# Performance work log

Hardware: AMD Instinct MI355X
Metric: run time of the kernel (lower is better)

The kernel has to match this reference:

```python
import jax, jax.numpy as jnp
import numpy as np

GAMMA = 0.99
EPS = 1e-8
N = 16777216  # flattened reward count


def setup_inputs() -> dict:
    key = jax.random.key(0)
    rewards = jax.random.normal(key, (N,), dtype=jnp.float32)
    return {"rewards": rewards}


def reference(rewards):
    # Sequential recurrence: R_t = gamma*R_{t-1} + r_t, Welford stats over R_t,
    # scaled[i] = r_i / max(std_t, eps), std_t = sqrt(var_sum/count) (1.0 if count < 2).
    flat = rewards.reshape(-1)

    def step(carry, r):
        R, cnt, mean, var_sum = carry
        R = GAMMA * R + r
        cnt = cnt + 1.0
        delta = R - mean
        mean = mean + delta / cnt
        var_sum = var_sum + delta * (R - mean)
        std = jnp.where(cnt < 2.0, jnp.float32(1.0), jnp.sqrt(var_sum / cnt))
        std = jnp.maximum(std, jnp.float32(EPS))
        return (R, cnt, mean, var_sum), r / std

    init = (jnp.float32(0.0), jnp.float32(0.0), jnp.float32(0.0), jnp.float32(0.0))
    _, scaled = jax.lax.scan(step, init, flat)
    return scaled.reshape(rewards.shape)
```

## Files before the change

kernel.cpp:

```cpp
#include <hip/hip_runtime.h>
#include <math.h>

#define THREADS 256
#define GAMMA 0.99

typedef float vf4 __attribute__((ext_vector_type(4)));

__device__ __forceinline__ int padi16(int i) { return i + (i >> 4); }

template<int NW>
__device__ __forceinline__ void block_compose_excl(int tid, double g, double v,
                                                   double& eg, double& ev,
                                                   double* lg, double* lv) {
    const int lane = tid & 63, wave = tid >> 6;
    double ig = g, iv = v;
#pragma unroll
    for (int k = 1; k < 64; k <<= 1) {
        double og = __shfl_up(ig, k);
        double ov = __shfl_up(iv, k);
        if (lane >= k) { iv = fma(ig, ov, iv); ig *= og; }
    }
    double weg = __shfl_up(ig, 1);
    double wev = __shfl_up(iv, 1);
    if (lane == 0) { weg = 1.0; wev = 0.0; }
    if (lane == 63) { lg[wave] = ig; lv[wave] = iv; }
    __syncthreads();
    double bg = 1.0, bv = 0.0;
    for (int w = 0; w < wave; ++w) { bv = fma(lg[w], bv, lv[w]); bg *= lg[w]; }
    eg = weg * bg;
    ev = fma(weg, bv, wev);
}

template<int NW>
__device__ __forceinline__ void block_add_excl2(int tid, double a, double b,
                                                double& ea, double& eb,
                                                double* la, double* lb) {
    const int lane = tid & 63, wave = tid >> 6;
    double ia = a, ib = b;
#pragma unroll
    for (int k = 1; k < 64; k <<= 1) {
        double oa = __shfl_up(ia, k);
        double ob = __shfl_up(ib, k);
        if (lane >= k) { ia += oa; ib += ob; }
    }
    double wea = __shfl_up(ia, 1);
    double web = __shfl_up(ib, 1);
    if (lane == 0) { wea = 0.0; web = 0.0; }
    if (lane == 63) { la[wave] = ia; lb[wave] = ib; }
    __syncthreads();
    double ba = 0.0, bb = 0.0;
    for (int w = 0; w < wave; ++w) { ba += la[w]; bb += lb[w]; }
    ea = wea + ba;
    eb = web + bb;
}


__global__ __launch_bounds__(THREADS) void w_phase1(const float* __restrict__ in,
                                                    vf4* __restrict__ aggf,
                                                    double* __restrict__ bagg, int nw) {
    __shared__ double sA[4], sPs[4], sPq[4], sP2[4];
    const int tid = threadIdx.x, lane = tid & 63, w = tid >> 6;
    const int wid = blockIdx.x * 4 + w;

    const float* src = in + (size_t)wid * 1024 + (size_t)lane * 16;
    float rv[16];
#pragma unroll
    for (int q = 0; q < 4; ++q) {
        const float4 t = ((const float4*)src)[q];
        rv[4 * q] = t.x; rv[4 * q + 1] = t.y; rv[4 * q + 2] = t.z; rv[4 * q + 3] = t.w;
    }
    const float gf = (float)GAMMA;
    float p = 0.f, psum = 0.f, pq = 0.f, p2 = 0.f, gp = 1.f;
#pragma unroll
    for (int j = 0; j < 16; ++j) {
        p = fmaf(gf, p, rv[j]);
        gp *= gf;
        psum += p;
        pq = fmaf(gp, p, pq);
        p2 = fmaf(p, p, p2);
    }
    const double g = GAMMA;
    double gPT = g;
#pragma unroll
    for (int e = 0; e < 4; ++e) gPT *= gPT;

    float ig = (float)gPT, iv = p;
#pragma unroll
    for (int k = 1; k < 64; k <<= 1) {
        float og = __shfl_up(ig, k);
        float ov = __shfl_up(iv, k);
        if (lane >= k) { iv = fmaf(ig, ov, iv); ig *= og; }
    }
    float rho = __shfl_up(iv, 1), gexc = __shfl_up(ig, 1);
    if (lane == 0) { rho = 0.f; gexc = 1.f; }
    const float A = __shfl(iv, 63);

    const float G1f = (float)(g * (1.0 - gPT) / (1.0 - g));
    const float G2f = (float)(g * g * (1.0 - gPT * gPT) / (1.0 - g * g));
    float c1 = fmaf(rho, G1f, psum);
    float c2 = gexc * fmaf(rho, G2f, pq);
    float c3 = fmaf(rho * rho, G2f, fmaf(2.f * rho, pq, p2));
#pragma unroll
    for (int k = 32; k > 0; k >>= 1) {
        c1 += __shfl_down(c1, k);
        c2 += __shfl_down(c2, k);
        c3 += __shfl_down(c3, k);
    }
    if (lane == 0) {
        vf4 a; a.x = A; a.y = c1; a.z = c2; a.w = c3;
        aggf[wid] = a;
        sA[w] = (double)A; sPs[w] = (double)c1; sPq[w] = (double)c2; sP2[w] = (double)c3;
    }
    __syncthreads();
    if (tid == 0) {
        double gC = g;
#pragma unroll
        for (int e = 0; e < 10; ++e) gC *= gC;
        const double G1C = g * (1.0 - gC) / (1.0 - g);
        const double G2C = g * g * (1.0 - gC * gC) / (1.0 - g * g);
        double Rin = 0.0, Ps = 0.0, Pq = 0.0, P2 = 0.0, gex = 1.0;
#pragma unroll
        for (int i = 0; i < 4; ++i) {
            Ps += fma(Rin, G1C, sPs[i]);
            Pq += gex * fma(Rin, G2C, sPq[i]);
            P2 += fma(Rin * Rin, G2C, fma(2.0 * Rin, sPq[i], sP2[i]));
            Rin = fma(gC, Rin, sA[i]);
            gex *= gC;
        }
        bagg[4 * (size_t)blockIdx.x + 0] = Rin;
        bagg[4 * (size_t)blockIdx.x + 1] = Ps;
        bagg[4 * (size_t)blockIdx.x + 2] = Pq;
        bagg[4 * (size_t)blockIdx.x + 3] = P2;
    }
}

template<int CPT, int LOG2CHUNK>
__global__ __launch_bounds__(1024) void rs_phase2(const double* __restrict__ agg,
                                                  double* __restrict__ car, int nchunk) {
    __shared__ double lg[16], lv[16], la[16], lb[16];
    const int t = threadIdx.x;
    const double g = GAMMA;
    double gC = g;
#pragma unroll
    for (int e = 0; e < LOG2CHUNK; ++e) gC *= gC;

    double A[CPT], Ps[CPT], Pq[CPT], P2[CPT];
    const int c0 = t * CPT;
#pragma unroll
    for (int i = 0; i < CPT; ++i) {
        const int c = c0 + i;
        const bool ok = c < nchunk;
        A[i]  = ok ? agg[4 * (size_t)c + 0] : 0.0;
        Ps[i] = ok ? agg[4 * (size_t)c + 1] : 0.0;
        Pq[i] = ok ? agg[4 * (size_t)c + 2] : 0.0;
        P2[i] = ok ? agg[4 * (size_t)c + 3] : 0.0;
    }
    double mg = 1.0, mv = 0.0;
#pragma unroll
    for (int i = 0; i < CPT; ++i) { mv = fma(gC, mv, A[i]); mg *= gC; }

    double eg, ev;
    block_compose_excl<16>(t, mg, mv, eg, ev, lg, lv);

    const double G1C = g * (1.0 - gC) / (1.0 - g);
    const double G2C = g * g * (1.0 - gC * gC) / (1.0 - g * g);
    double Rin[CPT + 1];
    Rin[0] = ev;
    double s1[CPT], s2[CPT];
#pragma unroll
    for (int i = 0; i < CPT; ++i) {
        s1[i] = fma(Rin[i], G1C, Ps[i]);
        s2[i] = fma(Rin[i] * Rin[i], G2C, fma(2.0 * Rin[i], Pq[i], P2[i]));
        Rin[i + 1] = fma(gC, Rin[i], A[i]);
    }
    double ts1 = 0.0, ts2 = 0.0;
#pragma unroll
    for (int i = 0; i < CPT; ++i) { ts1 += s1[i]; ts2 += s2[i]; }
    double ea, eb;
    block_add_excl2<16>(t, ts1, ts2, ea, eb, la, lb);
#pragma unroll
    for (int i = 0; i < CPT; ++i) {
        const int c = c0 + i;
        if (c < nchunk) {
            car[3 * (size_t)c + 0] = Rin[i];
            car[3 * (size_t)c + 1] = ea;
            car[3 * (size_t)c + 2] = eb;
        }
        ea += s1[i];
        eb += s2[i];
    }
}

__global__ __launch_bounds__(THREADS) void w_expand(const double* __restrict__ bcar,
                                                    const vf4* __restrict__ aggf,
                                                    double* __restrict__ wcar, int nc) {
    const int c = blockIdx.x * THREADS + threadIdx.x;
    if (c >= nc) return;
    const double g = GAMMA;
    double gW = g;
#pragma unroll
    for (int e = 0; e < 10; ++e) gW *= gW;
    const double G1W = g * (1.0 - gW) / (1.0 - g);
    const double G2W = g * g * (1.0 - gW * gW) / (1.0 - g * g);

    const vf4 a0 = aggf[4 * (size_t)c + 0];
    const vf4 a1 = aggf[4 * (size_t)c + 1];
    const vf4 a2 = aggf[4 * (size_t)c + 2];
    const vf4 a3 = aggf[4 * (size_t)c + 3];
    double wR  = bcar[3 * (size_t)c + 0];
    double wS1 = bcar[3 * (size_t)c + 1];
    double wS2 = bcar[3 * (size_t)c + 2];

    const vf4 aj[4] = {a0, a1, a2, a3};
#pragma unroll
    for (int j = 0; j < 4; ++j) {
        const size_t wd = 4 * (size_t)c + j;
        wcar[3 * wd + 0] = wR;
        wcar[3 * wd + 1] = wS1;
        wcar[3 * wd + 2] = wS2;
        const double Aw = (double)aj[j].x, Pw = (double)aj[j].y;
        const double Qw = (double)aj[j].z, Sw = (double)aj[j].w;
        wS1 += fma(wR, G1W, Pw);
        wS2 += fma(wR * wR, G2W, fma(2.0 * wR, Qw, Sw));
        wR = fma(gW, wR, Aw);
    }
}

__global__ __launch_bounds__(THREADS) void w_phase3(const float* __restrict__ in,
                                                    float* __restrict__ out,
                                                    const double* __restrict__ wcar, int nw) {
    __shared__ float sbuf[THREADS / 64][1024 + 64];
    const int tid = threadIdx.x, lane = tid & 63, w = tid >> 6;
    const int wid = blockIdx.x * 4 + w;

    const double RinC = wcar[3 * (size_t)wid + 0];
    const double S1C  = wcar[3 * (size_t)wid + 1];
    const double S2C  = wcar[3 * (size_t)wid + 2];

    const float* src = in + (size_t)wid * 1024 + (size_t)lane * 16;
    float rv[16];
#pragma unroll
    for (int q = 0; q < 4; ++q) {
        const float4 t = ((const float4*)src)[q];
        rv[4 * q] = t.x; rv[4 * q + 1] = t.y; rv[4 * q + 2] = t.z; rv[4 * q + 3] = t.w;
    }
    const float gf = (float)GAMMA;
    float p = 0.f, psum = 0.f, pq = 0.f, p2 = 0.f, gp = 1.f;
#pragma unroll
    for (int j = 0; j < 16; ++j) {
        p = fmaf(gf, p, rv[j]);
        gp *= gf;
        psum += p;
        pq = fmaf(gp, p, pq);
        p2 = fmaf(p, p, p2);
    }
    const double g = GAMMA;
    double gPT = g;
#pragma unroll
    for (int e = 0; e < 4; ++e) gPT *= gPT;

    if (wid == 0) {
        double ig = gPT, iv = (double)p;
#pragma unroll
        for (int k = 1; k < 64; k <<= 1) {
            double og = __shfl_up(ig, k);
            double ov = __shfl_up(iv, k);
            if (lane >= k) { iv = fma(ig, ov, iv); ig *= og; }
        }
        double rho = __shfl_up(iv, 1), gexc = __shfl_up(ig, 1);
        if (lane == 0) { rho = 0.0; gexc = 1.0; }
        const double rin = fma(gexc, RinC, rho);
        const double G1 = g * (1.0 - gPT) / (1.0 - g);
        const double G2 = g * g * (1.0 - gPT * gPT) / (1.0 - g * g);
        double s1 = fma(rin, G1, (double)psum);
        double s2 = fma(rin * rin, G2, fma(2.0 * rin, (double)pq, (double)p2));
        double ia = s1, ib = s2;
#pragma unroll
        for (int k = 1; k < 64; k <<= 1) {
            double oa = __shfl_up(ia, k);
            double ob = __shfl_up(ib, k);
            if (lane >= k) { ia += oa; ib += ob; }
        }
        double ea = __shfl_up(ia, 1), eb = __shfl_up(ib, 1);
        if (lane == 0) { ea = 0.0; eb = 0.0; }
        double R = rin, S1 = S1C + ea, S2 = S2C + eb;
        const int a0 = lane * 17;
        const size_t gbase = (size_t)lane * 16;
        for (int j = 0; j < 16; ++j) {
            const float rf = rv[j];
            R = fma(g, R, (double)rf);
            S1 += R;
            S2 = fma(R, R, S2);
            float ov;
            if (gbase + j == 0) {
                ov = rf;
            } else {
                const double cnt = (double)(gbase + j + 1);
                const double inv = 1.0 / cnt;
                const double mean = S1 * inv;
                double var = fma(S2, inv, -(mean * mean));
                var = var > 0.0 ? var : 0.0;
                double sd = sqrt(var);
                sd = sd > 1e-8 ? sd : 1e-8;
                ov = (float)((double)rf / sd);
            }
            sbuf[w][a0 + j] = ov;
        }
    } else {
        float ig = (float)gPT, iv = p;
#pragma unroll
        for (int k = 1; k < 64; k <<= 1) {
            float og = __shfl_up(ig, k);
            float ov = __shfl_up(iv, k);
            if (lane >= k) { iv = fmaf(ig, ov, iv); ig *= og; }
        }
        float rho = __shfl_up(iv, 1), gexc = __shfl_up(ig, 1);
        if (lane == 0) { rho = 0.f; gexc = 1.f; }
        const float rin = fmaf(gexc, (float)RinC, rho);
        const float G1f = (float)(g * (1.0 - gPT) / (1.0 - g));
        const float G2f = (float)(g * g * (1.0 - gPT * gPT) / (1.0 - g * g));
        float s1 = fmaf(rin, G1f, psum);
        float s2 = fmaf(rin * rin, G2f, fmaf(2.f * rin, pq, p2));
        float ia = s1, ib = s2;
#pragma unroll
        for (int k = 1; k < 64; k <<= 1) {
            float oa = __shfl_up(ia, k);
            float ob = __shfl_up(ib, k);
            if (lane >= k) { ia += oa; ib += ob; }
        }
        float ea = __shfl_up(ia, 1), eb = __shfl_up(ib, 1);
        if (lane == 0) { ea = 0.f; eb = 0.f; }
        const float S1bf = (float)S1C + ea;
        const float S2bf = (float)S2C + eb;

        float R = rin;
        float ls1 = 0.f, ls2 = 0.f;
        const float base_cnt = (float)((size_t)wid * 1024 + (size_t)lane * 16);
        const int a0 = lane * 17;
#pragma unroll
        for (int j = 0; j < 16; ++j) {
            const float rf = rv[j];
            R = fmaf(gf, R, rf);
            ls1 += R;
            ls2 = fmaf(R, R, ls2);
            const float cnt = base_cnt + (float)(j + 1);
            const float S1f = S1bf + ls1;
            const float S2f = S2bf + ls2;
            float t = fmaf(S2f, cnt, -(S1f * S1f));
            t = fmaxf(t, 1e-12f);
            sbuf[w][a0 + j] = rf * cnt * __builtin_amdgcn_rsqf(t);
        }
    }

    asm volatile("s_waitcnt lgkmcnt(0)" ::: "memory");

    float* dst = out + (size_t)wid * 1024;
#pragma unroll
    for (int k = 0; k < 4; ++k) {
        const int i = lane * 4 + k * 256;
        const int pp = padi16(i);
        vf4 v;
        v.x = sbuf[w][pp]; v.y = sbuf[w][pp + 1]; v.z = sbuf[w][pp + 2]; v.w = sbuf[w][pp + 3];
        __builtin_nontemporal_store(v, (vf4*)(dst + i));
    }
}

extern "C" void kernel_launch(void* const* d_in, const int* in_sizes, int n_in,
                              void* d_out, int out_size, void* d_ws, size_t ws_size,
                              hipStream_t stream) {
    (void)n_in; (void)out_size; (void)ws_size;
    const float* in = (const float*)d_in[0];
    float* out = (float*)d_out;
    double* ws = (double*)d_ws;
    const int n = in_sizes[0];

    const int nw = n >> 10;
    const int nc = nw >> 2;
    double* bagg = ws;
    double* bcar = bagg + 4 * (size_t)nc;
    double* wcar = bcar + 3 * (size_t)nc;
    vf4* aggf = (vf4*)(wcar + 3 * (size_t)nw);

    w_phase1<<<nc, THREADS, 0, stream>>>(in, aggf, bagg, nw);
    rs_phase2<4, 12><<<1, 1024, 0, stream>>>(bagg, bcar, nc);
    w_expand<<<(nc + THREADS - 1) / THREADS, THREADS, 0, stream>>>(bcar, aggf, wcar, nc);
    w_phase3<<<nc, THREADS, 0, stream>>>(in, out, wcar, nw);
}
```

Measured before the change: 53.71 us.

## Fold warp-carry expansion into phase3 and move first-warp exact path to phase1

```diff
diff --git a/kernel.cpp b/kernel.cpp
--- a/kernel.cpp
+++ b/kernel.cpp
@@ -56,6 +56,7 @@
 
 
 __global__ __launch_bounds__(THREADS) void w_phase1(const float* __restrict__ in,
+                                                    float* __restrict__ out,
                                                     vf4* __restrict__ aggf,
                                                     double* __restrict__ bagg, int nw) {
     __shared__ double sA[4], sPs[4], sPq[4], sP2[4];
@@ -132,144 +133,17 @@
         bagg[4 * (size_t)blockIdx.x + 2] = Pq;
         bagg[4 * (size_t)blockIdx.x + 3] = P2;
     }
-}
-
-template<int CPT, int LOG2CHUNK>
-__global__ __launch_bounds__(1024) void rs_phase2(const double* __restrict__ agg,
-                                                  double* __restrict__ car, int nchunk) {
-    __shared__ double lg[16], lv[16], la[16], lb[16];
-    const int t = threadIdx.x;
-    const double g = GAMMA;
-    double gC = g;
-#pragma unroll
-    for (int e = 0; e < LOG2CHUNK; ++e) gC *= gC;
-
-    double A[CPT], Ps[CPT], Pq[CPT], P2[CPT];
-    const int c0 = t * CPT;
-#pragma unroll
-    for (int i = 0; i < CPT; ++i) {
-        const int c = c0 + i;
-        const bool ok = c < nchunk;
-        A[i]  = ok ? agg[4 * (size_t)c + 0] : 0.0;
-        Ps[i] = ok ? agg[4 * (size_t)c + 1] : 0.0;
-        Pq[i] = ok ? agg[4 * (size_t)c + 2] : 0.0;
-        P2[i] = ok ? agg[4 * (size_t)c + 3] : 0.0;
-    }
-    double mg = 1.0, mv = 0.0;
-#pragma unroll
-    for (int i = 0; i < CPT; ++i) { mv = fma(gC, mv, A[i]); mg *= gC; }
-
-    double eg, ev;
-    block_compose_excl<16>(t, mg, mv, eg, ev, lg, lv);
-
-    const double G1C = g * (1.0 - gC) / (1.0 - g);
-    const double G2C = g * g * (1.0 - gC * gC) / (1.0 - g * g);
-    double Rin[CPT + 1];
-    Rin[0] = ev;
-    double s1[CPT], s2[CPT];
-#pragma unroll
-    for (int i = 0; i < CPT; ++i) {
-        s1[i] = fma(Rin[i], G1C, Ps[i]);
-        s2[i] = fma(Rin[i] * Rin[i], G2C, fma(2.0 * Rin[i], Pq[i], P2[i]));
-        Rin[i + 1] = fma(gC, Rin[i], A[i]);
-    }
-    double ts1 = 0.0, ts2 = 0.0;
-#pragma unroll
-    for (int i = 0; i < CPT; ++i) { ts1 += s1[i]; ts2 += s2[i]; }
-    double ea, eb;
-    block_add_excl2<16>(t, ts1, ts2, ea, eb, la, lb);
-#pragma unroll
-    for (int i = 0; i < CPT; ++i) {
-        const int c = c0 + i;
-        if (c < nchunk) {
-            car[3 * (size_t)c + 0] = Rin[i];
-            car[3 * (size_t)c + 1] = ea;
-            car[3 * (size_t)c + 2] = eb;
-        }
-        ea += s1[i];
-        eb += s2[i];
-    }
-}
-
-__global__ __launch_bounds__(THREADS) void w_expand(const double* __restrict__ bcar,
-                                                    const vf4* __restrict__ aggf,
-                                                    double* __restrict__ wcar, int nc) {
-    const int c = blockIdx.x * THREADS + threadIdx.x;
-    if (c >= nc) return;
-    const double g = GAMMA;
-    double gW = g;
-#pragma unroll
-    for (int e = 0; e < 10; ++e) gW *= gW;
-    const double G1W = g * (1.0 - gW) / (1.0 - g);
-    const double G2W = g * g * (1.0 - gW * gW) / (1.0 - g * g);
-
-    const vf4 a0 = aggf[4 * (size_t)c + 0];
-    const vf4 a1 = aggf[4 * (size_t)c + 1];
-    const vf4 a2 = aggf[4 * (size_t)c + 2];
-    const vf4 a3 = aggf[4 * (size_t)c + 3];
-    double wR  = bcar[3 * (size_t)c + 0];
-    double wS1 = bcar[3 * (size_t)c + 1];
-    double wS2 = bcar[3 * (size_t)c + 2];
-
-    const vf4 aj[4] = {a0, a1, a2, a3};
-#pragma unroll
-    for (int j = 0; j < 4; ++j) {
-        const size_t wd = 4 * (size_t)c + j;
-        wcar[3 * wd + 0] = wR;
-        wcar[3 * wd + 1] = wS1;
-        wcar[3 * wd + 2] = wS2;
-        const double Aw = (double)aj[j].x, Pw = (double)aj[j].y;
-        const double Qw = (double)aj[j].z, Sw = (double)aj[j].w;
-        wS1 += fma(wR, G1W, Pw);
-        wS2 += fma(wR * wR, G2W, fma(2.0 * wR, Qw, Sw));
-        wR = fma(gW, wR, Aw);
-    }
-}
-
-__global__ __launch_bounds__(THREADS) void w_phase3(const float* __restrict__ in,
-                                                    float* __restrict__ out,
-                                                    const double* __restrict__ wcar, int nw) {
-    __shared__ float sbuf[THREADS / 64][1024 + 64];
-    const int tid = threadIdx.x, lane = tid & 63, w = tid >> 6;
-    const int wid = blockIdx.x * 4 + w;
-
-    const double RinC = wcar[3 * (size_t)wid + 0];
-    const double S1C  = wcar[3 * (size_t)wid + 1];
-    const double S2C  = wcar[3 * (size_t)wid + 2];
-
-    const float* src = in + (size_t)wid * 1024 + (size_t)lane * 16;
-    float rv[16];
-#pragma unroll
-    for (int q = 0; q < 4; ++q) {
-        const float4 t = ((const float4*)src)[q];
-        rv[4 * q] = t.x; rv[4 * q + 1] = t.y; rv[4 * q + 2] = t.z; rv[4 * q + 3] = t.w;
-    }
-    const float gf = (float)GAMMA;
-    float p = 0.f, psum = 0.f, pq = 0.f, p2 = 0.f, gp = 1.f;
-#pragma unroll
-    for (int j = 0; j < 16; ++j) {
-        p = fmaf(gf, p, rv[j]);
-        gp *= gf;
-        psum += p;
-        pq = fmaf(gp, p, pq);
-        p2 = fmaf(p, p, p2);
-    }
-    const double g = GAMMA;
-    double gPT = g;
-#pragma unroll
-    for (int e = 0; e < 4; ++e) gPT *= gPT;
-
-    if (wid == 0) {
-        double ig = gPT, iv = (double)p;
+
+    if (blockIdx.x == 0 && w == 0) {
+        double ig64 = gPT, iv64 = (double)p;
 #pragma unroll
         for (int k = 1; k < 64; k <<= 1) {
-            double og = __shfl_up(ig, k);
-            double ov = __shfl_up(iv, k);
-            if (lane >= k) { iv = fma(ig, ov, iv); ig *= og; }
-        }
-        double rho = __shfl_up(iv, 1), gexc = __shfl_up(ig, 1);
-        if (lane == 0) { rho = 0.0; gexc = 1.0; }
-        const double rin = fma(gexc, RinC, rho);
+            double og = __shfl_up(ig64, k);
+            double ov = __shfl_up(iv64, k);
+            if (lane >= k) { iv64 = fma(ig64, ov, iv64); ig64 *= og; }
+        }
+        double rin = __shfl_up(iv64, 1);
+        if (lane == 0) rin = 0.0;
         const double G1 = g * (1.0 - gPT) / (1.0 - g);
         const double G2 = g * g * (1.0 - gPT * gPT) / (1.0 - g * g);
         double s1 = fma(rin, G1, (double)psum);
@@ -283,8 +157,7 @@
         }
         double ea = __shfl_up(ia, 1), eb = __shfl_up(ib, 1);
         if (lane == 0) { ea = 0.0; eb = 0.0; }
-        double R = rin, S1 = S1C + ea, S2 = S2C + eb;
-        const int a0 = lane * 17;
+        double R = rin, S1 = ea, S2 = eb;
         const size_t gbase = (size_t)lane * 16;
         for (int j = 0; j < 16; ++j) {
             const float rf = rv[j];
@@ -304,52 +177,160 @@
                 sd = sd > 1e-8 ? sd : 1e-8;
                 ov = (float)((double)rf / sd);
             }
-            sbuf[w][a0 + j] = ov;
-        }
-    } else {
-        float ig = (float)gPT, iv = p;
-#pragma unroll
-        for (int k = 1; k < 64; k <<= 1) {
-            float og = __shfl_up(ig, k);
-            float ov = __shfl_up(iv, k);
-            if (lane >= k) { iv = fmaf(ig, ov, iv); ig *= og; }
-        }
-        float rho = __shfl_up(iv, 1), gexc = __shfl_up(ig, 1);
-        if (lane == 0) { rho = 0.f; gexc = 1.f; }
-        const float rin = fmaf(gexc, (float)RinC, rho);
-        const float G1f = (float)(g * (1.0 - gPT) / (1.0 - g));
-        const float G2f = (float)(g * g * (1.0 - gPT * gPT) / (1.0 - g * g));
-        float s1 = fmaf(rin, G1f, psum);
-        float s2 = fmaf(rin * rin, G2f, fmaf(2.f * rin, pq, p2));
-        float ia = s1, ib = s2;
-#pragma unroll
-        for (int k = 1; k < 64; k <<= 1) {
-            float oa = __shfl_up(ia, k);
-            float ob = __shfl_up(ib, k);
-            if (lane >= k) { ia += oa; ib += ob; }
-        }
-        float ea = __shfl_up(ia, 1), eb = __shfl_up(ib, 1);
-        if (lane == 0) { ea = 0.f; eb = 0.f; }
-        const float S1bf = (float)S1C + ea;
-        const float S2bf = (float)S2C + eb;
-
-        float R = rin;
-        float ls1 = 0.f, ls2 = 0.f;
-        const float base_cnt = (float)((size_t)wid * 1024 + (size_t)lane * 16);
-        const int a0 = lane * 17;
-#pragma unroll
-        for (int j = 0; j < 16; ++j) {
-            const float rf = rv[j];
-            R = fmaf(gf, R, rf);
-            ls1 += R;
-            ls2 = fmaf(R, R, ls2);
-            const float cnt = base_cnt + (float)(j + 1);
-            const float S1f = S1bf + ls1;
-            const float S2f = S2bf + ls2;
-            float t = fmaf(S2f, cnt, -(S1f * S1f));
-            t = fmaxf(t, 1e-12f);
-            sbuf[w][a0 + j] = rf * cnt * __builtin_amdgcn_rsqf(t);
-        }
+            out[gbase + j] = ov;
+        }
+    }
+}
+
+template<int CPT, int LOG2CHUNK>
+__global__ __launch_bounds__(1024) void rs_phase2(const double* __restrict__ agg,
+                                                  double* __restrict__ car, int nchunk) {
+    __shared__ double lg[16], lv[16], la[16], lb[16];
+    const int t = threadIdx.x;
+    const double g = GAMMA;
+    double gC = g;
+#pragma unroll
+    for (int e = 0; e < LOG2CHUNK; ++e) gC *= gC;
+
+    double A[CPT], Ps[CPT], Pq[CPT], P2[CPT];
+    const int c0 = t * CPT;
+#pragma unroll
+    for (int i = 0; i < CPT; ++i) {
+        const int c = c0 + i;
+        const bool ok = c < nchunk;
+        A[i]  = ok ? agg[4 * (size_t)c + 0] : 0.0;
+        Ps[i] = ok ? agg[4 * (size_t)c + 1] : 0.0;
+        Pq[i] = ok ? agg[4 * (size_t)c + 2] : 0.0;
+        P2[i] = ok ? agg[4 * (size_t)c + 3] : 0.0;
+    }
+    double mg = 1.0, mv = 0.0;
+#pragma unroll
+    for (int i = 0; i < CPT; ++i) { mv = fma(gC, mv, A[i]); mg *= gC; }
+
+    double eg, ev;
+    block_compose_excl<16>(t, mg, mv, eg, ev, lg, lv);
+
+    const double G1C = g * (1.0 - gC) / (1.0 - g);
+    const double G2C = g * g * (1.0 - gC * gC) / (1.0 - g * g);
+    double Rin[CPT + 1];
+    Rin[0] = ev;
+    double s1[CPT], s2[CPT];
+#pragma unroll
+    for (int i = 0; i < CPT; ++i) {
+        s1[i] = fma(Rin[i], G1C, Ps[i]);
+        s2[i] = fma(Rin[i] * Rin[i], G2C, fma(2.0 * Rin[i], Pq[i], P2[i]));
+        Rin[i + 1] = fma(gC, Rin[i], A[i]);
+    }
+    double ts1 = 0.0, ts2 = 0.0;
+#pragma unroll
+    for (int i = 0; i < CPT; ++i) { ts1 += s1[i]; ts2 += s2[i]; }
+    double ea, eb;
+    block_add_excl2<16>(t, ts1, ts2, ea, eb, la, lb);
+#pragma unroll
+    for (int i = 0; i < CPT; ++i) {
+        const int c = c0 + i;
+        if (c < nchunk) {
+            car[3 * (size_t)c + 0] = Rin[i];
+            car[3 * (size_t)c + 1] = ea;
+            car[3 * (size_t)c + 2] = eb;
+        }
+        ea += s1[i];
+        eb += s2[i];
+    }
+}
+
+__global__ __launch_bounds__(THREADS) void w_phase3(const float* __restrict__ in,
+                                                    float* __restrict__ out,
+                                                    const double* __restrict__ bcar,
+                                                    const vf4* __restrict__ aggf, int nw) {
+    __shared__ float sbuf[THREADS / 64][1024 + 64];
+    const int tid = threadIdx.x, lane = tid & 63, w = tid >> 6;
+    const int wid = blockIdx.x * 4 + w;
+    if (wid == 0) return;
+    const int b = blockIdx.x;
+
+    const float* src = in + (size_t)wid * 1024 + (size_t)lane * 16;
+    float rv[16];
+#pragma unroll
+    for (int q = 0; q < 4; ++q) {
+        const float4 t = ((const float4*)src)[q];
+        rv[4 * q] = t.x; rv[4 * q + 1] = t.y; rv[4 * q + 2] = t.z; rv[4 * q + 3] = t.w;
+    }
+
+    const double g = GAMMA;
+    double gW64 = g;
+#pragma unroll
+    for (int e = 0; e < 10; ++e) gW64 *= gW64;
+    const float gW  = (float)gW64;
+    const float G1W = (float)(g * (1.0 - gW64) / (1.0 - g));
+    const float G2W = (float)(g * g * (1.0 - gW64 * gW64) / (1.0 - g * g));
+
+    float Rc  = (float)bcar[3 * (size_t)b + 0];
+    float S1C = (float)bcar[3 * (size_t)b + 1];
+    float S2C = (float)bcar[3 * (size_t)b + 2];
+    for (int i = 0; i < w; ++i) {
+        const vf4 a = aggf[4 * (size_t)b + i];
+        S1C += fmaf(Rc, G1W, a.y);
+        S2C += fmaf(Rc * Rc, G2W, fmaf(2.f * Rc, a.z, a.w));
+        Rc = fmaf(gW, Rc, a.x);
+    }
+
+    const float gf = (float)GAMMA;
+    float p = 0.f, psum = 0.f, pq = 0.f, p2 = 0.f, gp = 1.f;
+#pragma unroll
+    for (int j = 0; j < 16; ++j) {
+        p = fmaf(gf, p, rv[j]);
+        gp *= gf;
+        psum += p;
+        pq = fmaf(gp, p, pq);
+        p2 = fmaf(p, p, p2);
+    }
+    double gPT64 = g;
+#pragma unroll
+    for (int e = 0; e < 4; ++e) gPT64 *= gPT64;
+
+    float ig = (float)gPT64, iv = p;
+#pragma unroll
+    for (int k = 1; k < 64; k <<= 1) {
+        float og = __shfl_up(ig, k);
+        float ov = __shfl_up(iv, k);
+        if (lane >= k) { iv = fmaf(ig, ov, iv); ig *= og; }
+    }
+    float rho = __shfl_up(iv, 1), gexc = __shfl_up(ig, 1);
+    if (lane == 0) { rho = 0.f; gexc = 1.f; }
+    const float rin = fmaf(gexc, Rc, rho);
+    const float G1f = (float)(g * (1.0 - gPT64) / (1.0 - g));
+    const float G2f = (float)(g * g * (1.0 - gPT64 * gPT64) / (1.0 - g * g));
+    float s1 = fmaf(rin, G1f, psum);
+    float s2 = fmaf(rin * rin, G2f, fmaf(2.f * rin, pq, p2));
+    float ia = s1, ib = s2;
+#pragma unroll
+    for (int k = 1; k < 64; k <<= 1) {
+        float oa = __shfl_up(ia, k);
+        float ob = __shfl_up(ib, k);
+        if (lane >= k) { ia += oa; ib += ob; }
+    }
+    float ea = __shfl_up(ia, 1), eb = __shfl_up(ib, 1);
+    if (lane == 0) { ea = 0.f; eb = 0.f; }
+    const float S1bf = S1C + ea;
+    const float S2bf = S2C + eb;
+
+    float R = rin;
+    float ls1 = 0.f, ls2 = 0.f;
+    const float base_cnt = (float)((size_t)wid * 1024 + (size_t)lane * 16);
+    const int a0 = lane * 17;
+#pragma unroll
+    for (int j = 0; j < 16; ++j) {
+        const float rf = rv[j];
+        R = fmaf(gf, R, rf);
+        ls1 += R;
+        ls2 = fmaf(R, R, ls2);
+        const float cnt = base_cnt + (float)(j + 1);
+        const float S1f = S1bf + ls1;
+        const float S2f = S2bf + ls2;
+        float t = fmaf(S2f, cnt, -(S1f * S1f));
+        t = fmaxf(t, 1e-12f);
+        sbuf[w][a0 + j] = rf * cnt * __builtin_amdgcn_rsqf(t);
     }
 
     asm volatile("s_waitcnt lgkmcnt(0)" ::: "memory");
@@ -378,11 +359,9 @@
     const int nc = nw >> 2;
     double* bagg = ws;
     double* bcar = bagg + 4 * (size_t)nc;
-    double* wcar = bcar + 3 * (size_t)nc;
-    vf4* aggf = (vf4*)(wcar + 3 * (size_t)nw);
-
-    w_phase1<<<nc, THREADS, 0, stream>>>(in, aggf, bagg, nw);
+    vf4* aggf = (vf4*)(bcar + 3 * (size_t)nc);
+
+    w_phase1<<<nc, THREADS, 0, stream>>>(in, out, aggf, bagg, nw);
     rs_phase2<4, 12><<<1, 1024, 0, stream>>>(bagg, bcar, nc);
-    w_expand<<<(nc + THREADS - 1) / THREADS, THREADS, 0, stream>>>(bcar, aggf, wcar, nc);
-    w_phase3<<<nc, THREADS, 0, stream>>>(in, out, wcar, nw);
-}
+    w_phase3<<<nc, THREADS, 0, stream>>>(in, out, bcar, aggf, nw);
+}
```

After: 51.15 us. -4.8%, faster.
